# Kernel optimization log

Measured on AMD Instinct MI355X. Metric: run time of the kernel, lower is better.

Reference implementation:

```python
import jax, jax.numpy as jnp
import numpy as np

D_MODEL = 1024
D_FF = 4096
NUM_EXPERTS = 8
TOP_K = 2
LN_EPS = 1e-5


def setup_inputs() -> dict:
    key = jax.random.key(0)
    ks = jax.random.split(key, 8)
    B, S = 4, 2048
    x = jax.random.normal(ks[0], (B, S, D_MODEL), dtype=jnp.float32)
    router_w = jax.random.normal(ks[1], (D_MODEL, NUM_EXPERTS), dtype=jnp.float32) * (1.0 / np.sqrt(D_MODEL))
    router_b = jnp.zeros((NUM_EXPERTS,), dtype=jnp.float32)
    w1 = jax.random.normal(ks[2], (NUM_EXPERTS, D_MODEL, D_FF), dtype=jnp.float32) * (1.0 / np.sqrt(D_MODEL))
    b1 = jnp.zeros((NUM_EXPERTS, D_FF), dtype=jnp.float32)
    w2 = jax.random.normal(ks[3], (NUM_EXPERTS, D_FF, D_MODEL), dtype=jnp.float32) * (1.0 / np.sqrt(D_FF))
    b2 = jnp.zeros((NUM_EXPERTS, D_MODEL), dtype=jnp.float32)
    gamma = jnp.ones((D_MODEL,), dtype=jnp.float32)
    beta = jnp.zeros((D_MODEL,), dtype=jnp.float32)
    return {"x": x, "router_w": router_w, "router_b": router_b,
            "w1": w1, "b1": b1, "w2": w2, "b2": b2,
            "gamma": gamma, "beta": beta}


def reference(x, router_w, router_b, w1, b1, w2, b2, gamma, beta):
    B, S, D = x.shape
    E = w1.shape[0]
    xf = x.reshape(B * S, D)  # [T, D]

    # Router: linear -> softmax -> top-k (scores are softmax probs of selected experts)
    logits = xf @ router_w + router_b                     # [T, E]
    probs = jax.nn.softmax(logits, axis=-1)
    scores, idx = jax.lax.top_k(probs, TOP_K)             # [T, K]

    # Dense combine weights: comb[t, e] = sum_k scores[t,k] * (idx[t,k]==e)
    comb = (jax.nn.one_hot(idx, E, dtype=x.dtype) * scores[..., None]).sum(axis=1)  # [T, E]

    # Dispatch/compute/combine. comb is 0 for unrouted (token, expert) pairs,
    # so the weighted sum matches the gather/scatter loop in the original.
    out = jnp.zeros_like(xf)
    for e in range(E):  # fixed small expert count, structurally distinct weights
        h = jax.nn.gelu(xf @ w1[e] + b1[e])               # [T, D_FF]
        out = out + comb[:, e:e + 1] * (h @ w2[e] + b2[e])
    out = out.reshape(B, S, D)

    # residual + LayerNorm (dropout = 0.0)
    y = x + out
    mu = y.mean(axis=-1, keepdims=True)
    var = ((y - mu) ** 2).mean(axis=-1, keepdims=True)
    z = (y - mu) * jax.lax.rsqrt(var + LN_EPS) * gamma + beta

    # routing decision export (bool mask over experts, jit-friendly stand-in for a Python set)
    selected = comb.sum(axis=0) > 0
    return z, selected
```

## Files before the change

kernel.cpp:

```cpp
#include <hip/hip_runtime.h>


#define T_TOKENS 8192
#define DM 1024
#define DF 4096
#define NE 8

typedef unsigned short u16;
typedef short v8s __attribute__((ext_vector_type(8)));
typedef float v4f __attribute__((ext_vector_type(4)));

__device__ __forceinline__ u16 f2bf(float f) {
  unsigned u = __float_as_uint(f);
  u += 0x7FFFu + ((u >> 16) & 1u);
  return (u16)(u >> 16);
}

__device__ __forceinline__ void load16_lds(const u16* g, u16* lds) {
  __builtin_amdgcn_global_load_lds(
      (const __attribute__((address_space(1))) unsigned int*)g,
      (__attribute__((address_space(3))) unsigned int*)lds, 16, 0, 0);
}

__global__ __launch_bounds__(256) void cvt_x_kernel(const float* __restrict__ x,
                                                    u16* __restrict__ xb) {
  size_t i = ((size_t)blockIdx.x * 256 + threadIdx.x) * 8;
  float4 v0 = *(const float4*)(x + i);
  float4 v1 = *(const float4*)(x + i + 4);
  int4 o;
  o.x = (int)f2bf(v0.x) | ((int)f2bf(v0.y) << 16);
  o.y = (int)f2bf(v0.z) | ((int)f2bf(v0.w) << 16);
  o.z = (int)f2bf(v1.x) | ((int)f2bf(v1.y) << 16);
  o.w = (int)f2bf(v1.z) | ((int)f2bf(v1.w) << 16);
  *(int4*)(xb + i) = o;
}

__global__ __launch_bounds__(64) void router_kernel(
    const float* __restrict__ x, const float* __restrict__ rw,
    const float* __restrict__ rb, int* __restrict__ counts,
    int* __restrict__ list_token, int* __restrict__ epos,
    float* __restrict__ escore) {
  int t = blockIdx.x;
  int lane = threadIdx.x;
  const float* xr = x + (size_t)t * DM;
  float a[8] = {0.f, 0.f, 0.f, 0.f, 0.f, 0.f, 0.f, 0.f};
  for (int j = lane; j < DM; j += 64) {
    float xv = xr[j];
    const float4* r4 = (const float4*)(rw + (size_t)j * 8);
    float4 w0 = r4[0], w1 = r4[1];
    a[0] += xv * w0.x; a[1] += xv * w0.y; a[2] += xv * w0.z; a[3] += xv * w0.w;
    a[4] += xv * w1.x; a[5] += xv * w1.y; a[6] += xv * w1.z; a[7] += xv * w1.w;
  }
#pragma unroll
  for (int e = 0; e < 8; e++)
#pragma unroll
    for (int off = 32; off > 0; off >>= 1) a[e] += __shfl_down(a[e], off);
  if (lane == 0) {
    float l[8];
    float mx = -1e30f;
#pragma unroll
    for (int e = 0; e < 8; e++) { l[e] = a[e] + rb[e]; mx = fmaxf(mx, l[e]); }
    float sum = 0.f;
#pragma unroll
    for (int e = 0; e < 8; e++) { l[e] = __expf(l[e] - mx); sum += l[e]; }
    float inv = 1.f / sum;
    int i1 = 0; float p1 = -1.f;
#pragma unroll
    for (int e = 0; e < 8; e++) if (l[e] > p1) { p1 = l[e]; i1 = e; }
    int i2 = -1; float p2 = -1.f;
#pragma unroll
    for (int e = 0; e < 8; e++) if (e != i1 && l[e] > p2) { p2 = l[e]; i2 = e; }
    int pos1 = atomicAdd(&counts[i1], 1);
    int pos2 = atomicAdd(&counts[i2], 1);
    list_token[i1 * T_TOKENS + pos1] = t;
    list_token[i2 * T_TOKENS + pos2] = t;
    epos[2 * t] = (i1 << 16) | pos1;
    epos[2 * t + 1] = (i2 << 16) | pos2;
    escore[2 * t] = p1 * inv;
    escore[2 * t + 1] = p2 * inv;
  }
}

__global__ __launch_bounds__(64) void finalize_kernel(const int* __restrict__ counts,
                                                      int* __restrict__ offsets,
                                                      float* __restrict__ sel_out) {
  int tid = threadIdx.x;
  if (tid == 0) {
    int o = 0;
    for (int e = 0; e < NE; e++) { offsets[e] = o; o += counts[e]; }
    offsets[NE] = o;
  }
  if (tid < NE) sel_out[tid] = counts[tid] > 0 ? 1.f : 0.f;
}

__global__ __launch_bounds__(256) void transpose_cvt_kernel(
    const float* __restrict__ src, u16* __restrict__ dst, int R, int C) {
  __shared__ float tile[64][33];
  int e = blockIdx.z;
  const float* s = src + (size_t)e * R * C;
  u16* d = dst + (size_t)e * R * C;
  int c0 = blockIdx.x * 32, r0 = blockIdx.y * 64;
  int tx = threadIdx.x, ty = threadIdx.y;
#pragma unroll
  for (int i = 0; i < 8; i++) {
    int r = r0 + ty + i * 8;
    tile[ty + i * 8][tx] = s[(size_t)r * C + c0 + tx];
  }
  __syncthreads();
#pragma unroll
  for (int i = 0; i < 4; i++) {
    int c = c0 + ty + i * 8;
    unsigned lo = f2bf(tile[2 * tx][ty + i * 8]);
    unsigned hi = f2bf(tile[2 * tx + 1][ty + i * 8]);
    *(unsigned*)&d[(size_t)c * R + r0 + 2 * tx] = lo | (hi << 16);
  }
}

__global__ __launch_bounds__(256) void gemm1_kernel(
    const u16* __restrict__ xb, const u16* __restrict__ w1t,
    const float* __restrict__ b1, const int* __restrict__ counts,
    const int* __restrict__ offsets, const int* __restrict__ list_token,
    u16* __restrict__ H) {
  int e = blockIdx.z;
  int cnt = counts[e];
  int r0 = blockIdx.y * 128;
  if (r0 >= cnt) return;
  int n0 = blockIdx.x * 128;
  int rem = cnt - r0;

  __shared__ __align__(16) u16 As[128 * 32];
  __shared__ __align__(16) u16 Bs[128 * 32];

  int tid = threadIdx.x;
  int ra0 = tid >> 2, ca0 = tid & 3;
  int ra1 = ra0 + 64, ca1 = ca0;
  const int* lst = list_token + e * T_TOKENS + r0;
  int tok0 = (ra0 < rem) ? lst[ra0] : lst[0];
  int tok1 = (ra1 < rem) ? lst[ra1] : lst[0];
  const u16* gA0 = xb + (size_t)tok0 * DM + ca0 * 8;
  const u16* gA1 = xb + (size_t)tok1 * DM + ca1 * 8;
  const u16* gB0 = w1t + ((size_t)e * DF + n0 + ra0) * DM + ca0 * 8;
  const u16* gB1 = w1t + ((size_t)e * DF + n0 + ra1) * DM + ca1 * 8;

  int lane = tid & 63, wv = tid >> 6;
  u16* ldsA0 = As + wv * 512;
  u16* ldsA1 = As + 2048 + wv * 512;
  u16* ldsB0 = Bs + wv * 512;
  u16* ldsB1 = Bs + 2048 + wv * 512;

  int wm = (wv >> 1) * 64, wn = (wv & 1) * 64;
  int ml = lane & 15, quad = lane >> 4;

  v4f acc[4][4];
#pragma unroll
  for (int i = 0; i < 4; i++)
#pragma unroll
    for (int j = 0; j < 4; j++) acc[i][j] = (v4f){0.f, 0.f, 0.f, 0.f};

  for (int k0 = 0; k0 < DM; k0 += 32) {
    load16_lds(gA0 + k0, ldsA0);
    load16_lds(gA1 + k0, ldsA1);
    load16_lds(gB0 + k0, ldsB0);
    load16_lds(gB1 + k0, ldsB1);
    __syncthreads();
    v8s af[4], bf[4];
#pragma unroll
    for (int i = 0; i < 4; i++)
      af[i] = *(const v8s*)&As[(wm + i * 16 + ml) * 32 + quad * 8];
#pragma unroll
    for (int j = 0; j < 4; j++)
      bf[j] = *(const v8s*)&Bs[(wn + j * 16 + ml) * 32 + quad * 8];
#pragma unroll
    for (int i = 0; i < 4; i++)
#pragma unroll
      for (int j = 0; j < 4; j++)
        acc[i][j] = __builtin_amdgcn_mfma_f32_16x16x32_bf16(af[i], bf[j], acc[i][j], 0, 0, 0);
    __syncthreads();
  }

  int slotbase = offsets[e] + r0;
#pragma unroll
  for (int i = 0; i < 4; i++) {
    int rbase = wm + i * 16 + quad * 4;
#pragma unroll
    for (int j = 0; j < 4; j++) {
      int cc = n0 + wn + j * 16 + ml;
      float bias = b1[e * DF + cc];
#pragma unroll
      for (int r = 0; r < 4; r++) {
        int row = rbase + r;
        if (row < rem) {
          float v = acc[i][j][r] + bias;
          float u = 0.7978845608028654f * (v + 0.044715f * v * v * v);
          float h = v / (1.f + __expf(-2.f * u));
          H[(size_t)(slotbase + row) * DF + cc] = f2bf(h);
        }
      }
    }
  }
}

__global__ __launch_bounds__(256) void gemm2_kernel(
    const u16* __restrict__ H, const u16* __restrict__ w2t,
    const float* __restrict__ b2, const int* __restrict__ counts,
    const int* __restrict__ offsets, float* __restrict__ partial) {
  int e = blockIdx.z;
  int cnt = counts[e];
  int r0 = blockIdx.y * 128;
  if (r0 >= cnt) return;
  int n0 = blockIdx.x * 128;
  int rem = cnt - r0;
  int slotbase = offsets[e] + r0;

  __shared__ __align__(16) u16 As[128 * 32];
  __shared__ __align__(16) u16 Bs[128 * 32];

  int tid = threadIdx.x;
  int ra0 = tid >> 2, ca0 = tid & 3;
  int ra1 = ra0 + 64, ca1 = ca0;
  int ar0 = (ra0 < rem) ? ra0 : 0;
  int ar1 = (ra1 < rem) ? ra1 : 0;
  const u16* gA0 = H + (size_t)(slotbase + ar0) * DF + ca0 * 8;
  const u16* gA1 = H + (size_t)(slotbase + ar1) * DF + ca1 * 8;
  const u16* gB0 = w2t + ((size_t)e * DM + n0 + ra0) * DF + ca0 * 8;
  const u16* gB1 = w2t + ((size_t)e * DM + n0 + ra1) * DF + ca1 * 8;

  int lane = tid & 63, wv = tid >> 6;
  u16* ldsA0 = As + wv * 512;
  u16* ldsA1 = As + 2048 + wv * 512;
  u16* ldsB0 = Bs + wv * 512;
  u16* ldsB1 = Bs + 2048 + wv * 512;

  int wm = (wv >> 1) * 64, wn = (wv & 1) * 64;
  int ml = lane & 15, quad = lane >> 4;

  v4f acc[4][4];
#pragma unroll
  for (int i = 0; i < 4; i++)
#pragma unroll
    for (int j = 0; j < 4; j++) acc[i][j] = (v4f){0.f, 0.f, 0.f, 0.f};

  for (int k0 = 0; k0 < DF; k0 += 32) {
    load16_lds(gA0 + k0, ldsA0);
    load16_lds(gA1 + k0, ldsA1);
    load16_lds(gB0 + k0, ldsB0);
    load16_lds(gB1 + k0, ldsB1);
    __syncthreads();
    v8s af[4], bf[4];
#pragma unroll
    for (int i = 0; i < 4; i++)
      af[i] = *(const v8s*)&As[(wm + i * 16 + ml) * 32 + quad * 8];
#pragma unroll
    for (int j = 0; j < 4; j++)
      bf[j] = *(const v8s*)&Bs[(wn + j * 16 + ml) * 32 + quad * 8];
#pragma unroll
    for (int i = 0; i < 4; i++)
#pragma unroll
      for (int j = 0; j < 4; j++)
        acc[i][j] = __builtin_amdgcn_mfma_f32_16x16x32_bf16(af[i], bf[j], acc[i][j], 0, 0, 0);
    __syncthreads();
  }

#pragma unroll
  for (int i = 0; i < 4; i++) {
    int rbase = wm + i * 16 + quad * 4;
#pragma unroll
    for (int j = 0; j < 4; j++) {
      int cc = n0 + wn + j * 16 + ml;
      float bias = b2[e * DM + cc];
#pragma unroll
      for (int r = 0; r < 4; r++) {
        int row = rbase + r;
        if (row < rem)
          partial[(size_t)(slotbase + row) * DM + cc] = acc[i][j][r] + bias;
      }
    }
  }
}

__global__ __launch_bounds__(256) void ln_kernel(
    const float* __restrict__ x, const float* __restrict__ partial,
    const int* __restrict__ offsets, const int* __restrict__ epos,
    const float* __restrict__ escore, const float* __restrict__ gamma,
    const float* __restrict__ beta, float* __restrict__ out) {
  int t = blockIdx.x;
  int tid = threadIdx.x;
  int e0p = epos[2 * t], e1p = epos[2 * t + 1];
  float s0 = escore[2 * t], s1 = escore[2 * t + 1];
  size_t row0 = (size_t)offsets[e0p >> 16] + (e0p & 0xFFFF);
  size_t row1 = (size_t)offsets[e1p >> 16] + (e1p & 0xFFFF);
  float4 xv = ((const float4*)(x + (size_t)t * DM))[tid];
  float4 p0 = ((const float4*)(partial + row0 * DM))[tid];
  float4 p1 = ((const float4*)(partial + row1 * DM))[tid];
  float4 y;
  y.x = xv.x + s0 * p0.x + s1 * p1.x;
  y.y = xv.y + s0 * p0.y + s1 * p1.y;
  y.z = xv.z + s0 * p0.z + s1 * p1.z;
  y.w = xv.w + s0 * p0.w + s1 * p1.w;
  float s = y.x + y.y + y.z + y.w;
  float ss = y.x * y.x + y.y * y.y + y.z * y.z + y.w * y.w;
#pragma unroll
  for (int off = 32; off > 0; off >>= 1) {
    s += __shfl_down(s, off);
    ss += __shfl_down(ss, off);
  }
  __shared__ float red[10];
  int wid = tid >> 6, lane = tid & 63;
  if (lane == 0) { red[wid] = s; red[4 + wid] = ss; }
  __syncthreads();
  if (tid == 0) {
    float S = red[0] + red[1] + red[2] + red[3];
    float SS = red[4] + red[5] + red[6] + red[7];
    float mu = S * (1.f / DM);
    float var = SS * (1.f / DM) - mu * mu;
    red[8] = mu;
    red[9] = rsqrtf(var + 1e-5f);
  }
  __syncthreads();
  float mu = red[8], rs = red[9];
  float4 g = ((const float4*)gamma)[tid];
  float4 b = ((const float4*)beta)[tid];
  float4 z;
  z.x = (y.x - mu) * rs * g.x + b.x;
  z.y = (y.y - mu) * rs * g.y + b.y;
  z.z = (y.z - mu) * rs * g.z + b.z;
  z.w = (y.w - mu) * rs * g.w + b.w;
  ((float4*)(out + (size_t)t * DM))[tid] = z;
}

extern "C" void kernel_launch(void* const* d_in, const int* in_sizes, int n_in,
                              void* d_out, int out_size, void* d_ws, size_t ws_size,
                              hipStream_t stream) {
  const float* x = (const float*)d_in[0];
  const float* rw = (const float*)d_in[1];
  const float* rb = (const float*)d_in[2];
  const float* w1 = (const float*)d_in[3];
  const float* b1 = (const float*)d_in[4];
  const float* w2 = (const float*)d_in[5];
  const float* b2 = (const float*)d_in[6];
  const float* gamma = (const float*)d_in[7];
  const float* beta = (const float*)d_in[8];
  float* out = (float*)d_out;

  char* ws = (char*)d_ws;
  int* counts = (int*)(ws + 0);
  int* offsets = (int*)(ws + 256);
  int* list_token = (int*)(ws + 4096);
  int* epos = (int*)(ws + 266240);
  float* escore = (float*)(ws + 331776);
  u16* xb = (u16*)(ws + 1048576);
  u16* w1t = (u16*)(ws + 17825792);
  u16* w2t = (u16*)(ws + 84934656);
  u16* H = (u16*)(ws + 152043520);
  float* partial = (float*)(ws + 286261248);

  hipMemsetAsync(counts, 0, NE * sizeof(int), stream);

  cvt_x_kernel<<<dim3(4096), dim3(256), 0, stream>>>(x, xb);
  router_kernel<<<dim3(T_TOKENS), dim3(64), 0, stream>>>(x, rw, rb, counts,
                                                         list_token, epos, escore);
  finalize_kernel<<<dim3(1), dim3(64), 0, stream>>>(
      counts, offsets, out + (size_t)T_TOKENS * DM);
  transpose_cvt_kernel<<<dim3(128, 16, NE), dim3(32, 8), 0, stream>>>(w1, w1t, DM, DF);
  transpose_cvt_kernel<<<dim3(32, 64, NE), dim3(32, 8), 0, stream>>>(w2, w2t, DF, DM);

  gemm1_kernel<<<dim3(DF / 128, 64, NE), dim3(256), 0, stream>>>(
      xb, w1t, b1, counts, offsets, list_token, H);
  gemm2_kernel<<<dim3(DM / 128, 64, NE), dim3(256), 0, stream>>>(
      H, w2t, b2, counts, offsets, partial);
  ln_kernel<<<dim3(T_TOKENS), dim3(256), 0, stream>>>(x, partial, offsets, epos,
                                                      escore, gamma, beta, out);
}
```

Before: 1.034 ms.

## Fuse MoE combine into gemm2 via atomic scatter with split-K

The bf16 conversion of x moves into the router kernel, removing a separate cast kernel. gemm2 now splits K in two, doubling grid blocks, and scatters score-weighted outputs straight into a per-token fp32 accumulator with atomicAdd. The LN kernel then reads one accumulated row instead of gathering two partial rows. gemm1 packs pairs of bf16 outputs into 32-bit stores using a lane shuffle. The cost is an extra memset of the accumulator, many fp32 global atomics, and a summation order that is no longer deterministic.

After: 1.188 ms. +14.9%, slower.

```diff
diff --git a/kernel.cpp b/kernel.cpp
--- a/kernel.cpp
+++ b/kernel.cpp
@@ -22,30 +22,19 @@
       (__attribute__((address_space(3))) unsigned int*)lds, 16, 0, 0);
 }
 
-__global__ __launch_bounds__(256) void cvt_x_kernel(const float* __restrict__ x,
-                                                    u16* __restrict__ xb) {
-  size_t i = ((size_t)blockIdx.x * 256 + threadIdx.x) * 8;
-  float4 v0 = *(const float4*)(x + i);
-  float4 v1 = *(const float4*)(x + i + 4);
-  int4 o;
-  o.x = (int)f2bf(v0.x) | ((int)f2bf(v0.y) << 16);
-  o.y = (int)f2bf(v0.z) | ((int)f2bf(v0.w) << 16);
-  o.z = (int)f2bf(v1.x) | ((int)f2bf(v1.y) << 16);
-  o.w = (int)f2bf(v1.z) | ((int)f2bf(v1.w) << 16);
-  *(int4*)(xb + i) = o;
-}
-
 __global__ __launch_bounds__(64) void router_kernel(
     const float* __restrict__ x, const float* __restrict__ rw,
     const float* __restrict__ rb, int* __restrict__ counts,
-    int* __restrict__ list_token, int* __restrict__ epos,
-    float* __restrict__ escore) {
+    int* __restrict__ list_token, float* __restrict__ sscore,
+    u16* __restrict__ xb) {
   int t = blockIdx.x;
   int lane = threadIdx.x;
   const float* xr = x + (size_t)t * DM;
+  u16* xbr = xb + (size_t)t * DM;
   float a[8] = {0.f, 0.f, 0.f, 0.f, 0.f, 0.f, 0.f, 0.f};
   for (int j = lane; j < DM; j += 64) {
     float xv = xr[j];
+    xbr[j] = f2bf(xv);
     const float4* r4 = (const float4*)(rw + (size_t)j * 8);
     float4 w0 = r4[0], w1 = r4[1];
     a[0] += xv * w0.x; a[1] += xv * w0.y; a[2] += xv * w0.z; a[3] += xv * w0.w;
@@ -74,10 +63,8 @@
     int pos2 = atomicAdd(&counts[i2], 1);
     list_token[i1 * T_TOKENS + pos1] = t;
     list_token[i2 * T_TOKENS + pos2] = t;
-    epos[2 * t] = (i1 << 16) | pos1;
-    epos[2 * t + 1] = (i2 << 16) | pos2;
-    escore[2 * t] = p1 * inv;
-    escore[2 * t + 1] = p2 * inv;
+    sscore[i1 * T_TOKENS + pos1] = p1 * inv;
+    sscore[i2 * T_TOKENS + pos2] = p2 * inv;
   }
 }
 
@@ -133,14 +120,14 @@
 
   int tid = threadIdx.x;
   int ra0 = tid >> 2, ca0 = tid & 3;
-  int ra1 = ra0 + 64, ca1 = ca0;
+  int ra1 = ra0 + 64;
   const int* lst = list_token + e * T_TOKENS + r0;
   int tok0 = (ra0 < rem) ? lst[ra0] : lst[0];
   int tok1 = (ra1 < rem) ? lst[ra1] : lst[0];
   const u16* gA0 = xb + (size_t)tok0 * DM + ca0 * 8;
-  const u16* gA1 = xb + (size_t)tok1 * DM + ca1 * 8;
+  const u16* gA1 = xb + (size_t)tok1 * DM + ca0 * 8;
   const u16* gB0 = w1t + ((size_t)e * DF + n0 + ra0) * DM + ca0 * 8;
-  const u16* gB1 = w1t + ((size_t)e * DF + n0 + ra1) * DM + ca1 * 8;
+  const u16* gB1 = w1t + ((size_t)e * DF + n0 + ra1) * DM + ca0 * 8;
 
   int lane = tid & 63, wv = tid >> 6;
   u16* ldsA0 = As + wv * 512;
@@ -189,11 +176,13 @@
 #pragma unroll
       for (int r = 0; r < 4; r++) {
         int row = rbase + r;
-        if (row < rem) {
-          float v = acc[i][j][r] + bias;
-          float u = 0.7978845608028654f * (v + 0.044715f * v * v * v);
-          float h = v / (1.f + __expf(-2.f * u));
-          H[(size_t)(slotbase + row) * DF + cc] = f2bf(h);
+        float v = acc[i][j][r] + bias;
+        float u = 0.7978845608028654f * (v + 0.044715f * v * v * v);
+        float h = v / (1.f + __expf(-2.f * u));
+        float hp = __shfl_xor(h, 1);
+        if (((ml & 1) == 0) && row < rem) {
+          unsigned pk = (unsigned)f2bf(h) | ((unsigned)f2bf(hp) << 16);
+          *(unsigned*)&H[(size_t)(slotbase + row) * DF + cc] = pk;
         }
       }
     }
@@ -203,10 +192,12 @@
 __global__ __launch_bounds__(256) void gemm2_kernel(
     const u16* __restrict__ H, const u16* __restrict__ w2t,
     const float* __restrict__ b2, const int* __restrict__ counts,
-    const int* __restrict__ offsets, float* __restrict__ partial) {
+    const int* __restrict__ offsets, const int* __restrict__ list_token,
+    const float* __restrict__ sscore, float* __restrict__ acc_out) {
   int e = blockIdx.z;
   int cnt = counts[e];
-  int r0 = blockIdx.y * 128;
+  int kh = blockIdx.y & 1;
+  int r0 = (blockIdx.y >> 1) * 128;
   if (r0 >= cnt) return;
   int n0 = blockIdx.x * 128;
   int rem = cnt - r0;
@@ -217,13 +208,13 @@
 
   int tid = threadIdx.x;
   int ra0 = tid >> 2, ca0 = tid & 3;
-  int ra1 = ra0 + 64, ca1 = ca0;
+  int ra1 = ra0 + 64;
   int ar0 = (ra0 < rem) ? ra0 : 0;
   int ar1 = (ra1 < rem) ? ra1 : 0;
   const u16* gA0 = H + (size_t)(slotbase + ar0) * DF + ca0 * 8;
-  const u16* gA1 = H + (size_t)(slotbase + ar1) * DF + ca1 * 8;
+  const u16* gA1 = H + (size_t)(slotbase + ar1) * DF + ca0 * 8;
   const u16* gB0 = w2t + ((size_t)e * DM + n0 + ra0) * DF + ca0 * 8;
-  const u16* gB1 = w2t + ((size_t)e * DM + n0 + ra1) * DF + ca1 * 8;
+  const u16* gB1 = w2t + ((size_t)e * DM + n0 + ra1) * DF + ca0 * 8;
 
   int lane = tid & 63, wv = tid >> 6;
   u16* ldsA0 = As + wv * 512;
@@ -240,7 +231,8 @@
 #pragma unroll
     for (int j = 0; j < 4; j++) acc[i][j] = (v4f){0.f, 0.f, 0.f, 0.f};
 
-  for (int k0 = 0; k0 < DF; k0 += 32) {
+  int kbase = kh * (DF / 2);
+  for (int k0 = kbase; k0 < kbase + DF / 2; k0 += 32) {
     load16_lds(gA0 + k0, ldsA0);
     load16_lds(gA1 + k0, ldsA1);
     load16_lds(gB0 + k0, ldsB0);
@@ -261,42 +253,43 @@
     __syncthreads();
   }
 
+  const int* lst = list_token + e * T_TOKENS + r0;
+  const float* ssc = sscore + e * T_TOKENS + r0;
 #pragma unroll
   for (int i = 0; i < 4; i++) {
     int rbase = wm + i * 16 + quad * 4;
 #pragma unroll
-    for (int j = 0; j < 4; j++) {
-      int cc = n0 + wn + j * 16 + ml;
-      float bias = b2[e * DM + cc];
-#pragma unroll
-      for (int r = 0; r < 4; r++) {
-        int row = rbase + r;
-        if (row < rem)
-          partial[(size_t)(slotbase + row) * DM + cc] = acc[i][j][r] + bias;
+    for (int r = 0; r < 4; r++) {
+      int row = rbase + r;
+      if (row < rem) {
+        int tok = lst[row];
+        float sc = ssc[row];
+        float* dst = acc_out + (size_t)tok * DM;
+#pragma unroll
+        for (int j = 0; j < 4; j++) {
+          int cc = n0 + wn + j * 16 + ml;
+          float v = acc[i][j][r];
+          if (kh == 0) v += b2[e * DM + cc];
+          atomicAdd(dst + cc, sc * v);
+        }
       }
     }
   }
 }
 
 __global__ __launch_bounds__(256) void ln_kernel(
-    const float* __restrict__ x, const float* __restrict__ partial,
-    const int* __restrict__ offsets, const int* __restrict__ epos,
-    const float* __restrict__ escore, const float* __restrict__ gamma,
-    const float* __restrict__ beta, float* __restrict__ out) {
+    const float* __restrict__ x, const float* __restrict__ acc_in,
+    const float* __restrict__ gamma, const float* __restrict__ beta,
+    float* __restrict__ out) {
   int t = blockIdx.x;
   int tid = threadIdx.x;
-  int e0p = epos[2 * t], e1p = epos[2 * t + 1];
-  float s0 = escore[2 * t], s1 = escore[2 * t + 1];
-  size_t row0 = (size_t)offsets[e0p >> 16] + (e0p & 0xFFFF);
-  size_t row1 = (size_t)offsets[e1p >> 16] + (e1p & 0xFFFF);
   float4 xv = ((const float4*)(x + (size_t)t * DM))[tid];
-  float4 p0 = ((const float4*)(partial + row0 * DM))[tid];
-  float4 p1 = ((const float4*)(partial + row1 * DM))[tid];
+  float4 av = ((const float4*)(acc_in + (size_t)t * DM))[tid];
   float4 y;
-  y.x = xv.x + s0 * p0.x + s1 * p1.x;
-  y.y = xv.y + s0 * p0.y + s1 * p1.y;
-  y.z = xv.z + s0 * p0.z + s1 * p1.z;
-  y.w = xv.w + s0 * p0.w + s1 * p1.w;
+  y.x = xv.x + av.x;
+  y.y = xv.y + av.y;
+  y.z = xv.z + av.z;
+  y.w = xv.w + av.w;
   float s = y.x + y.y + y.z + y.w;
   float ss = y.x * y.x + y.y * y.y + y.z * y.z + y.w * y.w;
 #pragma unroll
@@ -346,19 +339,18 @@
   int* counts = (int*)(ws + 0);
   int* offsets = (int*)(ws + 256);
   int* list_token = (int*)(ws + 4096);
-  int* epos = (int*)(ws + 266240);
-  float* escore = (float*)(ws + 331776);
+  float* sscore = (float*)(ws + 266240);
   u16* xb = (u16*)(ws + 1048576);
   u16* w1t = (u16*)(ws + 17825792);
   u16* w2t = (u16*)(ws + 84934656);
   u16* H = (u16*)(ws + 152043520);
-  float* partial = (float*)(ws + 286261248);
+  float* acc = (float*)(ws + 286261248);
 
   hipMemsetAsync(counts, 0, NE * sizeof(int), stream);
-
-  cvt_x_kernel<<<dim3(4096), dim3(256), 0, stream>>>(x, xb);
+  hipMemsetAsync(acc, 0, (size_t)T_TOKENS * DM * sizeof(float), stream);
+
   router_kernel<<<dim3(T_TOKENS), dim3(64), 0, stream>>>(x, rw, rb, counts,
-                                                         list_token, epos, escore);
+                                                         list_token, sscore, xb);
   finalize_kernel<<<dim3(1), dim3(64), 0, stream>>>(
       counts, offsets, out + (size_t)T_TOKENS * DM);
   transpose_cvt_kernel<<<dim3(128, 16, NE), dim3(32, 8), 0, stream>>>(w1, w1t, DM, DF);
@@ -366,8 +358,7 @@
 
   gemm1_kernel<<<dim3(DF / 128, 64, NE), dim3(256), 0, stream>>>(
       xb, w1t, b1, counts, offsets, list_token, H);
-  gemm2_kernel<<<dim3(DM / 128, 64, NE), dim3(256), 0, stream>>>(
-      H, w2t, b2, counts, offsets, partial);
-  ln_kernel<<<dim3(T_TOKENS), dim3(256), 0, stream>>>(x, partial, offsets, epos,
-                                                      escore, gamma, beta, out);
-}
+  gemm2_kernel<<<dim3(DM / 128, 128, NE), dim3(256), 0, stream>>>(
+      H, w2t, b2, counts, offsets, list_token, sscore, acc);
+  ln_kernel<<<dim3(T_TOKENS), dim3(256), 0, stream>>>(x, acc, gamma, beta, out);
+}
```
